# Performance work log

Hardware: AMD Instinct MI355X
Metric: run time of the kernel (lower is better)

## Reference

```python
import jax, jax.numpy as jnp
import numpy as np

TAU = 0.2        # temperature
LAM = 0.5        # lambda_weight
P = 128          # proj_dim


def l2n(x):
    # tf.math.l2_normalize semantics: x / sqrt(max(sum(x^2), eps))
    return x / jnp.sqrt(jnp.maximum(jnp.sum(x * x, axis=-1, keepdims=True), 1e-12))


def global_head(feat, W1, b1, W2, b2):
    # GlobalAveragePooling2D -> Dense(2048, relu) -> Dense(128); dropout is identity in eval
    g = jnp.mean(feat, axis=(1, 2))                       # [B, C]
    return jax.nn.relu(g @ W1 + b1) @ W2 + b2             # [B, 128]


def dense_head(feat, W1, b1, W2, b2):
    # 1x1 Conv2D(2048, relu) -> 1x1 Conv2D(128) == per-pixel matmuls
    h = jax.nn.relu(jnp.einsum('bhwc,cd->bhwd', feat, W1) + b1)
    return jnp.einsum('bhwd,de->bhwe', h, W2) + b2        # [B, H, W, 128]


def dense_correspondence(q, k):
    b, h, w, c = q.shape
    f1 = q.reshape(b, h * w, c)
    f2 = k.reshape(b, h * w, c)
    sim = jnp.einsum('bnc,bmc->bnm', f1, f2)              # [B, hw, hw]
    idx = jnp.argmax(sim, axis=-1)                        # [B, hw]
    return jnp.take_along_axis(f2, idx[:, :, None], axis=1)  # batched gather


def info_nce(q, k):
    logits = (q @ k.T) / TAU                              # [N, N]
    lse = jax.nn.logsumexp(logits, axis=-1)
    pos = jnp.diagonal(logits)                            # labels = arange(N)
    return jnp.mean(lse - pos)


def queue_info_nce(q, k, queue):
    l_pos = jnp.sum(q * k, axis=-1, keepdims=True)        # [B, 1]
    l_neg = q @ queue.T                                   # [B, Q]
    logits = jnp.concatenate([l_pos, l_neg], axis=1) / TAU
    # labels are all zero -> positive logit is column 0
    return jnp.mean(jax.nn.logsumexp(logits, axis=-1) - logits[:, 0])


def setup_inputs() -> dict:
    key = jax.random.key(0)
    ks = jax.random.split(key, 16)
    B, H, W, C, D = 8, 28, 28, 1024, 2048
    Q = 65536
    s1 = 0.02
    inp = {
        'feat_q': jax.random.normal(ks[0], (B, H, W, C), jnp.float32),
        'feat_k': jax.random.normal(ks[1], (B, H, W, C), jnp.float32),
        'Wg1': jax.random.normal(ks[2], (C, D), jnp.float32) * s1,
        'bg1': jnp.zeros((D,), jnp.float32),
        'Wg2': jax.random.normal(ks[3], (D, P), jnp.float32) * s1,
        'bg2': jnp.zeros((P,), jnp.float32),
        'Wd1': jax.random.normal(ks[4], (C, D), jnp.float32) * s1,
        'bd1': jnp.zeros((D,), jnp.float32),
        'Wd2': jax.random.normal(ks[5], (D, P), jnp.float32) * s1,
        'bd2': jnp.zeros((P,), jnp.float32),
        'mWg1': jax.random.normal(ks[6], (C, D), jnp.float32) * s1,
        'mbg1': jnp.zeros((D,), jnp.float32),
        'mWg2': jax.random.normal(ks[7], (D, P), jnp.float32) * s1,
        'mbg2': jnp.zeros((P,), jnp.float32),
        'mWd1': jax.random.normal(ks[8], (C, D), jnp.float32) * s1,
        'mbd1': jnp.zeros((D,), jnp.float32),
        'mWd2': jax.random.normal(ks[9], (D, P), jnp.float32) * s1,
        'mbd2': jnp.zeros((P,), jnp.float32),
        'queue': l2n(jax.random.normal(ks[10], (Q, P), jnp.float32)),
    }
    return inp


def reference(feat_q, feat_k, Wg1, bg1, Wg2, bg2, Wd1, bd1, Wd2, bd2,
              mWg1, mbg1, mWg2, mbg2, mWd1, mbd1, mWd2, mbd2, queue):
    # student branch
    q_g = l2n(global_head(feat_q, Wg1, bg1, Wg2, bg2))
    q_d = l2n(dense_head(feat_q, Wd1, bd1, Wd2, bd2))
    # momentum (teacher) branch, stop-gradient as in train_step
    k_g = jax.lax.stop_gradient(l2n(global_head(feat_k, mWg1, mbg1, mWg2, mbg2)))
    k_d = jax.lax.stop_gradient(l2n(dense_head(feat_k, mWd1, mbd1, mWd2, mbd2)))
    # post-warmup path (warmup_epochs=0)
    l_g = queue_info_nce(q_g, k_g, queue)
    matched_k = dense_correspondence(q_d, k_d)
    l_d = info_nce(q_d.reshape(-1, P), matched_k.reshape(-1, P))
    total = (1.0 - LAM) * l_g + LAM * l_d
    return total
```

## Files before the change

### kernel.cpp

```cpp
#include <hip/hip_runtime.h>
#include <cstdint>

#define TAU_INV 5.0f
#define L2E 1.4426950408889634f

using ushort = unsigned short;
typedef __attribute__((ext_vector_type(8))) short s16x8;
typedef __attribute__((ext_vector_type(4))) float f32x4;

static __device__ __forceinline__ ushort f2bf(float x) {
  unsigned u = __float_as_uint(x);
  return (ushort)((u + 0x7fffu + ((u >> 16) & 1u)) >> 16);
}

static __device__ __forceinline__ float fexp2(float x) {
#if __has_builtin(__builtin_amdgcn_exp2f)
  return __builtin_amdgcn_exp2f(x);
#else
  return exp2f(x);
#endif
}

static __device__ __forceinline__ void gload_lds16(const void* g, void* l) {
  __builtin_amdgcn_global_load_lds(
      reinterpret_cast<const __attribute__((address_space(1))) void*>(
          reinterpret_cast<uintptr_t>(g)),
      reinterpret_cast<__attribute__((address_space(3))) void*>(
          (unsigned)reinterpret_cast<uintptr_t>(l)),
      16, 0, 0);
}

static __device__ __forceinline__ void xcd_swizzle(int gx, int gy, int& bx, int& by) {
  int nwg = gx * gy;
  int flat = by * gx + bx;
  int q = nwg >> 3, r = nwg & 7;
  int xcd = flat & 7, sl = flat >> 3;
  int tile = (xcd < r ? xcd * (q + 1) : r * (q + 1) + (xcd - r) * q) + sl;
  by = tile / gx;
  bx = tile - by * gx;
}

__global__ void k_cvt_pool(const float* __restrict__ feat, ushort* __restrict__ obf,
                           float* __restrict__ gpart) {
  int b = blockIdx.y, pc = blockIdx.x, t = threadIdx.x;
  const float* fp = feat + ((size_t)b * 784 + (size_t)pc * 7) * 1024;
  ushort* op = obf + ((size_t)b * 784 + (size_t)pc * 7) * 1024;
  float4 acc = {0.f, 0.f, 0.f, 0.f};
#pragma unroll
  for (int p = 0; p < 7; ++p) {
    float4 v = ((const float4*)(fp + (size_t)p * 1024))[t];
    acc.x += v.x; acc.y += v.y; acc.z += v.z; acc.w += v.w;
    ushort4 r;
    r.x = f2bf(v.x); r.y = f2bf(v.y); r.z = f2bf(v.z); r.w = f2bf(v.w);
    ((ushort4*)(op + (size_t)p * 1024))[t] = r;
  }
  ((float4*)(gpart + ((size_t)b * 112 + pc) * 1024))[t] = acc;
}

__global__ void k_gpool_fin(const float* __restrict__ gpart, float* __restrict__ g) {
  int idx = blockIdx.x * 256 + threadIdx.x;
  int b = idx >> 10, c = idx & 1023;
  float s = 0.f;
#pragma unroll 4
  for (int pc = 0; pc < 112; ++pc) s += gpart[((size_t)b * 112 + pc) * 1024 + c];
  g[idx] = s * (1.0f / 784.0f);
}

__global__ void k_dense1_part(const float* __restrict__ g, const float* __restrict__ W,
                              float* __restrict__ part1) {
  int d = blockIdx.x * 256 + threadIdx.x;
  int k0 = blockIdx.y * 64;
  __shared__ float gs[512];
  for (int i = threadIdx.x; i < 512; i += 256) gs[i] = g[(i >> 6) * 1024 + k0 + (i & 63)];
  __syncthreads();
  float acc[8] = {};
  for (int kk = 0; kk < 64; ++kk) {
    float w = W[(size_t)(k0 + kk) * 2048 + d];
#pragma unroll
    for (int b = 0; b < 8; ++b) acc[b] += gs[b * 64 + kk] * w;
  }
#pragma unroll
  for (int b = 0; b < 8; ++b) part1[((size_t)blockIdx.y * 8 + b) * 2048 + d] = acc[b];
}

__global__ void k_dense1_fin(const float* __restrict__ part1, const float* __restrict__ bias,
                             float* __restrict__ h) {
  int idx = blockIdx.x * 256 + threadIdx.x;
  int b = idx >> 11, d = idx & 2047;
  float s = bias[d];
#pragma unroll
  for (int ks = 0; ks < 16; ++ks) s += part1[((size_t)ks * 8 + b) * 2048 + d];
  h[idx] = fmaxf(s, 0.f);
}

__global__ void k_dense2_part(const float* __restrict__ h, const float* __restrict__ W2,
                              float* __restrict__ part2) {
  int d = threadIdx.x;
  int k0 = blockIdx.x * 64;
  __shared__ float hs[512];
  for (int i = threadIdx.x; i < 512; i += 128) hs[i] = h[(i >> 6) * 2048 + k0 + (i & 63)];
  __syncthreads();
  float acc[8] = {};
  for (int kk = 0; kk < 64; ++kk) {
    float w = W2[(size_t)(k0 + kk) * 128 + d];
#pragma unroll
    for (int b = 0; b < 8; ++b) acc[b] += hs[b * 64 + kk] * w;
  }
#pragma unroll
  for (int b = 0; b < 8; ++b) part2[((size_t)blockIdx.x * 8 + b) * 128 + d] = acc[b];
}

__global__ void k_head_fin(const float* __restrict__ p2q, const float* __restrict__ p2k,
                           const float* __restrict__ bq, const float* __restrict__ bk,
                           float* __restrict__ qg, float* __restrict__ kg,
                           float* __restrict__ lpos) {
  int b = blockIdx.x, lane = threadIdx.x;
  float q0 = bq[lane], q1 = bq[lane + 64];
  float k0 = bk[lane], k1 = bk[lane + 64];
#pragma unroll
  for (int s = 0; s < 32; ++s) {
    size_t base = ((size_t)s * 8 + b) * 128;
    q0 += p2q[base + lane]; q1 += p2q[base + lane + 64];
    k0 += p2k[base + lane]; k1 += p2k[base + lane + 64];
  }
  float sq = q0 * q0 + q1 * q1, sk = k0 * k0 + k1 * k1;
#pragma unroll
  for (int d = 1; d < 64; d <<= 1) { sq += __shfl_xor(sq, d); sk += __shfl_xor(sk, d); }
  float rq = 1.0f / sqrtf(fmaxf(sq, 1e-12f));
  float rk = 1.0f / sqrtf(fmaxf(sk, 1e-12f));
  q0 *= rq; q1 *= rq; k0 *= rk; k1 *= rk;
  qg[b * 128 + lane] = q0; qg[b * 128 + 64 + lane] = q1;
  kg[b * 128 + lane] = k0; kg[b * 128 + 64 + lane] = k1;
  float lp = q0 * k0 + q1 * k1;
#pragma unroll
  for (int d = 1; d < 64; d <<= 1) lp += __shfl_xor(lp, d);
  if (lane == 0) lpos[b] = lp;
}

__global__ void k_transpose_cvt(const float* __restrict__ W, ushort* __restrict__ Wt, int K, int N) {
  __shared__ float tile[32][33];
  int n0 = blockIdx.x * 32, k0 = blockIdx.y * 32;
  int tx = threadIdx.x & 31, ty = threadIdx.x >> 5;
#pragma unroll
  for (int i = 0; i < 32; i += 8)
    tile[ty + i][tx] = W[(size_t)(k0 + ty + i) * N + n0 + tx];
  __syncthreads();
#pragma unroll
  for (int i = 0; i < 32; i += 8)
    Wt[(size_t)(n0 + ty + i) * K + k0 + tx] = f2bf(tile[tx][ty + i]);
}

template <int EPI>
__global__ __launch_bounds__(256) void k_gemm_abt(
    const ushort* __restrict__ A, const ushort* __restrict__ B,
    const float* __restrict__ bias, void* __restrict__ o0, void* __restrict__ o1,
    int Mvalid, int Nvalid, int Kloop, int lda, int ldb, int ldOut, int ntiles,
    float scale, long sA, long sB) {
  __shared__ unsigned char smem[65536];
  const int tid = threadIdx.x;
  int bx = blockIdx.x, by = blockIdx.y;
  const int bz = blockIdx.z;
  xcd_swizzle(gridDim.x, gridDim.y, bx, by);
  const ushort* Ab = A + (size_t)bz * sA;
  const ushort* Bb = B + (size_t)bz * sB;
  const int mBase = by * 128, nBase = bx * 128;
  const int lane = tid & 63;
  const int wid = tid >> 6;
  const int wid_u = __builtin_amdgcn_readfirstlane(wid);
  const int wm = wid >> 1, wn = wid & 1;
  const int lg = lane >> 4, li = lane & 15;
  const int lrow = lane >> 3, lchunk = lane & 7;

  const ushort* aSrc[4];
  const ushort* bSrc[4];
  int ldsOff[4];
#pragma unroll
  for (int j = 0; j < 4; ++j) {
    int r = wid_u * 32 + j * 8 + lrow;
    int gc = (lchunk ^ lrow) << 3;
    int ga = mBase + r; ga = ga < Mvalid ? ga : Mvalid - 1;
    int gb = nBase + r; gb = gb < Nvalid ? gb : Nvalid - 1;
    aSrc[j] = Ab + (size_t)ga * lda + gc;
    bSrc[j] = Bb + (size_t)gb * ldb + gc;
    ldsOff[j] = (wid_u * 32 + j * 8) * 128;
  }
  f32x4 acc[4][4] = {};

  auto STAGE = [&](int buf, int k0) {
    unsigned base = (unsigned)buf * 32768u;
#pragma unroll
    for (int j = 0; j < 4; ++j) {
      gload_lds16(aSrc[j] + k0, smem + base + ldsOff[j]);
      gload_lds16(bSrc[j] + k0, smem + base + 16384 + ldsOff[j]);
    }
  };

  const int nt = Kloop >> 6;
  STAGE(0, 0);
  __syncthreads();
  for (int t = 0; t < nt; ++t) {
    if (t + 1 < nt) STAGE((t + 1) & 1, (t + 1) << 6);
    const unsigned char* As = smem + (t & 1) * 32768;
    const unsigned char* Bs = As + 16384;
#pragma unroll
    for (int ks = 0; ks < 2; ++ks) {
      s16x8 af[4], bfr[4];
#pragma unroll
      for (int mi = 0; mi < 4; ++mi) {
        int r = wm * 64 + mi * 16 + li;
        af[mi] = *(const s16x8*)(const void*)(As + r * 128 + ((ks * 64 + lg * 16) ^ ((r & 7) << 4)));
      }
#pragma unroll
      for (int ni = 0; ni < 4; ++ni) {
        int c = wn * 64 + ni * 16 + li;
        bfr[ni] = *(const s16x8*)(const void*)(Bs + c * 128 + ((ks * 64 + lg * 16) ^ ((c & 7) << 4)));
      }
#pragma unroll
      for (int mi = 0; mi < 4; ++mi)
#pragma unroll
        for (int ni = 0; ni < 4; ++ni)
          acc[mi][ni] = __builtin_amdgcn_mfma_f32_16x16x32_bf16(af[mi], bfr[ni], acc[mi][ni], 0, 0, 0);
    }
    __syncthreads();
  }

  if constexpr (EPI == 0 || EPI == 4) {
    bool full = (mBase + 128 <= Mvalid) && (nBase + 128 <= Nvalid);
    if (full) {
#pragma unroll
      for (int ni = 0; ni < 4; ++ni) {
        int c = nBase + wn * 64 + ni * 16 + li;
        float bv = (EPI == 0) ? bias[c] : 0.f;
#pragma unroll
        for (int mi = 0; mi < 4; ++mi) {
#pragma unroll
          for (int rg = 0; rg < 4; ++rg) {
            int r = mBase + wm * 64 + mi * 16 + lg * 4 + rg;
            if constexpr (EPI == 0) {
              float v = fmaxf(acc[mi][ni][rg] + bv, 0.f);
              ((ushort*)o0)[(size_t)r * ldOut + c] = f2bf(v);
            } else {
              ((float*)o0)[(size_t)bz * ntiles + (size_t)r * ldOut + c] = acc[mi][ni][rg];
            }
          }
        }
      }
    } else {
#pragma unroll
      for (int mi = 0; mi < 4; ++mi)
#pragma unroll
        for (int ni = 0; ni < 4; ++ni) {
          int c = nBase + wn * 64 + ni * 16 + li;
#pragma unroll
          for (int rg = 0; rg < 4; ++rg) {
            int r = mBase + wm * 64 + mi * 16 + lg * 4 + rg;
            if (r < Mvalid && c < Nvalid) {
              if constexpr (EPI == 0) {
                float v = fmaxf(acc[mi][ni][rg] + bias[c], 0.f);
                ((ushort*)o0)[(size_t)r * ldOut + c] = f2bf(v);
              } else {
                ((float*)o0)[(size_t)bz * ntiles + (size_t)r * ldOut + c] = acc[mi][ni][rg];
              }
            }
          }
        }
    }
  } else if constexpr (EPI == 2) {
    __syncthreads();
    float* reds = (float*)(void*)smem;
#pragma unroll
    for (int mi = 0; mi < 4; ++mi)
#pragma unroll
      for (int rg = 0; rg < 4; ++rg) {
        float s = fexp2(acc[mi][0][rg] * scale) + fexp2(acc[mi][1][rg] * scale) +
                  fexp2(acc[mi][2][rg] * scale) + fexp2(acc[mi][3][rg] * scale);
#pragma unroll
        for (int d = 1; d < 16; d <<= 1) s += __shfl_xor(s, d);
        int rl = wm * 64 + mi * 16 + lg * 4 + rg;
        if (li == 0) reds[rl * 2 + wn] = s;
      }
    __syncthreads();
    if (tid < 128) {
      size_t idx = (size_t)(mBase + tid) * ntiles + bx;
      ((float*)o0)[idx] = reds[tid * 2] + reds[tid * 2 + 1];
    }
  } else if constexpr (EPI == 3) {
    __syncthreads();
    float* redv = (float*)(void*)smem;
    int* redi = (int*)(void*)(smem + 1024);
#pragma unroll
    for (int mi = 0; mi < 4; ++mi)
#pragma unroll
      for (int rg = 0; rg < 4; ++rg) {
        float bv = -3.4e38f;
        int bi = 0x7fffffff;
#pragma unroll
        for (int ni = 0; ni < 4; ++ni) {
          int c = nBase + wn * 64 + ni * 16 + li;
          float v = (c < Nvalid) ? acc[mi][ni][rg] : -3.4e38f;
          if (v > bv || (v == bv && c < bi)) { bv = v; bi = c; }
        }
#pragma unroll
        for (int d = 1; d < 16; d <<= 1) {
          float ov = __shfl_xor(bv, d);
          int oi = __shfl_xor(bi, d);
          if (ov > bv || (ov == bv && oi < bi)) { bv = ov; bi = oi; }
        }
        int rl = wm * 64 + mi * 16 + lg * 4 + rg;
        if (li == 0) { redv[rl * 2 + wn] = bv; redi[rl * 2 + wn] = bi; }
      }
    __syncthreads();
    if (tid < 128) {
      int r = mBase + tid;
      if (r < Mvalid) {
        float v0 = redv[tid * 2], v1 = redv[tid * 2 + 1];
        int i0 = redi[tid * 2], i1 = redi[tid * 2 + 1];
        float v = v0; int bi2 = i0;
        if (v1 > v || (v1 == v && i1 < bi2)) { v = v1; bi2 = i1; }
        size_t idx = (size_t)(bz * Mvalid + r) * ntiles + bx;
        ((float*)o0)[idx] = v;
        ((int*)o1)[idx] = bi2;
      }
    }
  }
}

__global__ void k_l2n_rows(const float* __restrict__ part, const float* __restrict__ bias,
                           float* __restrict__ of, ushort* __restrict__ ob, int rows) {
  int row = blockIdx.x * 4 + (threadIdx.x >> 6);
  int lane = threadIdx.x & 63;
  if (row >= rows) return;
  size_t i0 = (size_t)row * 128 + lane;
  const size_t SL = 802816;
  float v0 = bias[lane]      + part[i0]      + part[SL + i0]      + part[2 * SL + i0]      + part[3 * SL + i0];
  float v1 = bias[lane + 64] + part[i0 + 64] + part[SL + i0 + 64] + part[2 * SL + i0 + 64] + part[3 * SL + i0 + 64];
  float ss = v0 * v0 + v1 * v1;
#pragma unroll
  for (int d = 1; d < 64; d <<= 1) ss += __shfl_xor(ss, d);
  float r = 1.0f / sqrtf(fmaxf(ss, 1e-12f));
  of[i0] = v0 * r;
  of[i0 + 64] = v1 * r;
  ob[i0] = f2bf(v0 * r);
  ob[i0 + 64] = f2bf(v1 * r);
}

__global__ void k_argmax_gather(const float* __restrict__ pval, const int* __restrict__ pidx,
                                const ushort* __restrict__ kd_bf, ushort* __restrict__ matched_bf,
                                int* __restrict__ idxf) {
  int n = blockIdx.x;
  int b = n / 784;
  float bv = pval[(size_t)n * 7];
  int bi = pidx[(size_t)n * 7];
#pragma unroll
  for (int t = 1; t < 7; ++t) {
    float v = pval[(size_t)n * 7 + t];
    int i2 = pidx[(size_t)n * 7 + t];
    if (v > bv) { bv = v; bi = i2; }
  }
  int lane = threadIdx.x;
  if (lane == 0) idxf[n] = bi;
  const ushort* src = kd_bf + (size_t)(b * 784 + bi) * 128;
  ushort* dst = matched_bf + (size_t)n * 128;
  dst[lane] = src[lane];
  dst[lane + 64] = src[lane + 64];
}

__global__ __launch_bounds__(256) void k_queue_nce(const float* __restrict__ queue,
                                                   const float* __restrict__ qg,
                                                   float* __restrict__ ps) {
  __shared__ float qs[1024];
  int tid = threadIdx.x;
  for (int i = tid; i < 1024; i += 256) qs[i] = qg[i];
  __syncthreads();
  int r = blockIdx.x * 256 + tid;
  const float* qr = queue + (size_t)r * 128;
  float a[8] = {0, 0, 0, 0, 0, 0, 0, 0};
  for (int j = 0; j < 128; j += 4) {
    float4 v = *(const float4*)(const void*)(qr + j);
#pragma unroll
    for (int b = 0; b < 8; ++b)
      a[b] += v.x * qs[b * 128 + j] + v.y * qs[b * 128 + j + 1] +
              v.z * qs[b * 128 + j + 2] + v.w * qs[b * 128 + j + 3];
  }
  __shared__ float lssum[8][4];
  int lane = tid & 63, w = tid >> 6;
#pragma unroll
  for (int b = 0; b < 8; ++b) {
    float s = fexp2(a[b] * (TAU_INV * L2E));
#pragma unroll
    for (int d = 1; d < 64; d <<= 1) s += __shfl_xor(s, d);
    if (lane == 0) lssum[b][w] = s;
  }
  __syncthreads();
  if (tid < 8) {
    int b = tid;
    ps[blockIdx.x * 8 + b] = lssum[b][0] + lssum[b][1] + lssum[b][2] + lssum[b][3];
  }
}

__global__ void k_row_lse(const float* __restrict__ psum, const int* __restrict__ idxf,
                          const float* __restrict__ qd, const float* __restrict__ kd,
                          float* __restrict__ diff) {
  int n = blockIdx.x * 4 + (threadIdx.x >> 6);
  int lane = threadIdx.x & 63;
  float s = (lane < 49) ? psum[(size_t)n * 49 + lane] : 0.f;
#pragma unroll
  for (int d = 1; d < 64; d <<= 1) s += __shfl_xor(s, d);
  int b = n / 784;
  int mr = b * 784 + idxf[n];
  float pos = qd[(size_t)n * 128 + lane] * kd[(size_t)mr * 128 + lane] +
              qd[(size_t)n * 128 + 64 + lane] * kd[(size_t)mr * 128 + 64 + lane];
#pragma unroll
  for (int d = 1; d < 64; d <<= 1) pos += __shfl_xor(pos, d);
  if (lane == 0) diff[n] = logf(s) - pos * TAU_INV;
}

__global__ void k_final(const float* __restrict__ ps, const float* __restrict__ lpos,
                        const float* __restrict__ diff, float* __restrict__ out) {
  int tid = threadIdx.x;
  int lane = tid & 63, w = tid >> 6;
  __shared__ float sm[4];
  float lg = 0.f;
  for (int b = 0; b < 8; ++b) {
    float s = ps[tid * 8 + b];
#pragma unroll
    for (int d = 1; d < 64; d <<= 1) s += __shfl_xor(s, d);
    if (lane == 0) sm[w] = s;
    __syncthreads();
    if (tid == 0) {
      float S = sm[0] + sm[1] + sm[2] + sm[3];
      float lp = lpos[b] * TAU_INV;
      S += fexp2(lp * L2E);
      lg += logf(S) - lp;
    }
    __syncthreads();
  }
  float v = 0.f;
  for (int i = tid; i < 6272; i += 256) v += diff[i];
#pragma unroll
  for (int d = 1; d < 64; d <<= 1) v += __shfl_xor(v, d);
  if (lane == 0) sm[w] = v;
  __syncthreads();
  if (tid == 0) {
    float ld = sm[0] + sm[1] + sm[2] + sm[3];
    out[0] = 0.5f * (lg * 0.125f) + 0.5f * (ld * (1.0f / 6272.0f));
  }
}

extern "C" void kernel_launch(void* const* d_in, const int* in_sizes, int n_in,
                              void* d_out, int out_size, void* d_ws, size_t ws_size,
                              hipStream_t stream) {
  (void)in_sizes; (void)n_in; (void)out_size; (void)ws_size;
  const float* feat_q = (const float*)d_in[0];
  const float* feat_k = (const float*)d_in[1];
  const float* Wg1 = (const float*)d_in[2];
  const float* bg1 = (const float*)d_in[3];
  const float* Wg2 = (const float*)d_in[4];
  const float* bg2 = (const float*)d_in[5];
  const float* Wd1 = (const float*)d_in[6];
  const float* bd1 = (const float*)d_in[7];
  const float* Wd2 = (const float*)d_in[8];
  const float* bd2 = (const float*)d_in[9];
  const float* mWg1 = (const float*)d_in[10];
  const float* mbg1 = (const float*)d_in[11];
  const float* mWg2 = (const float*)d_in[12];
  const float* mbg2 = (const float*)d_in[13];
  const float* mWd1 = (const float*)d_in[14];
  const float* mbd1 = (const float*)d_in[15];
  const float* mWd2 = (const float*)d_in[16];
  const float* mbd2 = (const float*)d_in[17];
  const float* queue = (const float*)d_in[18];
  float* out = (float*)d_out;

  char* ws = (char*)d_ws;
  size_t off = 0;
  auto alloc = [&](size_t bytes) -> void* {
    void* p = (void*)(ws + off);
    off += (bytes + 255) & ~(size_t)255;
    return p;
  };

  ushort* featq_bf = (ushort*)alloc(6272ull * 1024 * 2);
  ushort* featk_bf = (ushort*)alloc(6272ull * 1024 * 2);
  ushort* Wd1t = (ushort*)alloc(2048ull * 1024 * 2);
  ushort* mWd1t = (ushort*)alloc(2048ull * 1024 * 2);
  ushort* Wd2t = (ushort*)alloc(128ull * 2048 * 2);
  ushort* mWd2t = (ushort*)alloc(128ull * 2048 * 2);
  ushort* h_bf = (ushort*)alloc(6272ull * 2048 * 2);
  float* e2part = (float*)alloc(4ull * 6272 * 128 * 4);
  float* qd = (float*)alloc(6272ull * 128 * 4);
  float* kd = (float*)alloc(6272ull * 128 * 4);
  ushort* qd_bf = (ushort*)alloc(6272ull * 128 * 2);
  ushort* kd_bf = (ushort*)alloc(6272ull * 128 * 2);
  ushort* matched_bf = (ushort*)alloc(6272ull * 128 * 2);
  float* psum = (float*)alloc(6272ull * 49 * 4);
  float* pval = (float*)alloc(6272ull * 7 * 4);
  int* pidx = (int*)alloc(6272ull * 7 * 4);
  int* idxf = (int*)alloc(6272ull * 4);
  float* gpart = (float*)alloc(8ull * 112 * 1024 * 4);
  float* gq = (float*)alloc(8ull * 1024 * 4);
  float* gk = (float*)alloc(8ull * 1024 * 4);
  float* part1 = (float*)alloc(16ull * 8 * 2048 * 4);
  float* hgq = (float*)alloc(8ull * 2048 * 4);
  float* hgk = (float*)alloc(8ull * 2048 * 4);
  float* part2q = (float*)alloc(32ull * 8 * 128 * 4);
  float* part2k = (float*)alloc(32ull * 8 * 128 * 4);
  float* qg = (float*)alloc(8ull * 128 * 4);
  float* kg = (float*)alloc(8ull * 128 * 4);
  float* l_pos = (float*)alloc(8ull * 4);
  float* qpart_s = (float*)alloc(256ull * 8 * 4);
  float* diff = (float*)alloc(6272ull * 4);

  k_cvt_pool<<<dim3(112, 8), 256, 0, stream>>>(feat_q, featq_bf, gpart);
  k_gpool_fin<<<32, 256, 0, stream>>>(gpart, gq);
  k_cvt_pool<<<dim3(112, 8), 256, 0, stream>>>(feat_k, featk_bf, gpart);
  k_gpool_fin<<<32, 256, 0, stream>>>(gpart, gk);

  k_transpose_cvt<<<dim3(64, 32), 256, 0, stream>>>(Wd1, Wd1t, 1024, 2048);
  k_transpose_cvt<<<dim3(64, 32), 256, 0, stream>>>(mWd1, mWd1t, 1024, 2048);
  k_transpose_cvt<<<dim3(4, 64), 256, 0, stream>>>(Wd2, Wd2t, 2048, 128);
  k_transpose_cvt<<<dim3(4, 64), 256, 0, stream>>>(mWd2, mWd2t, 2048, 128);

  k_dense1_part<<<dim3(8, 16), 256, 0, stream>>>(gq, Wg1, part1);
  k_dense1_fin<<<64, 256, 0, stream>>>(part1, bg1, hgq);
  k_dense2_part<<<32, 128, 0, stream>>>(hgq, Wg2, part2q);
  k_dense1_part<<<dim3(8, 16), 256, 0, stream>>>(gk, mWg1, part1);
  k_dense1_fin<<<64, 256, 0, stream>>>(part1, mbg1, hgk);
  k_dense2_part<<<32, 128, 0, stream>>>(hgk, mWg2, part2k);
  k_head_fin<<<8, 64, 0, stream>>>(part2q, part2k, bg2, mbg2, qg, kg, l_pos);

  k_gemm_abt<0><<<dim3(16, 49, 1), 256, 0, stream>>>(featq_bf, Wd1t, bd1, h_bf, nullptr,
                                                     6272, 2048, 1024, 1024, 1024, 2048, 0, 0.f, 0, 0);
  k_gemm_abt<4><<<dim3(1, 49, 4), 256, 0, stream>>>(h_bf, Wd2t, nullptr, e2part, nullptr,
                                                    6272, 128, 512, 2048, 2048, 128, 802816, 0.f, 512, 512);
  k_l2n_rows<<<1568, 256, 0, stream>>>(e2part, bd2, qd, qd_bf, 6272);

  k_gemm_abt<0><<<dim3(16, 49, 1), 256, 0, stream>>>(featk_bf, mWd1t, mbd1, h_bf, nullptr,
                                                     6272, 2048, 1024, 1024, 1024, 2048, 0, 0.f, 0, 0);
  k_gemm_abt<4><<<dim3(1, 49, 4), 256, 0, stream>>>(h_bf, mWd2t, nullptr, e2part, nullptr,
                                                    6272, 128, 512, 2048, 2048, 128, 802816, 0.f, 512, 512);
  k_l2n_rows<<<1568, 256, 0, stream>>>(e2part, mbd2, kd, kd_bf, 6272);

  k_gemm_abt<3><<<dim3(7, 7, 8), 256, 0, stream>>>(qd_bf, kd_bf, nullptr, pval, pidx,
                                                   784, 784, 128, 128, 128, 0, 7, 0.f,
                                                   784l * 128, 784l * 128);
  k_argmax_gather<<<6272, 64, 0, stream>>>(pval, pidx, kd_bf, matched_bf, idxf);

  k_gemm_abt<2><<<dim3(49, 49, 1), 256, 0, stream>>>(qd_bf, matched_bf, nullptr, psum, nullptr,
                                                     6272, 6272, 128, 128, 128, 0, 49,
                                                     TAU_INV * L2E, 0, 0);

  k_queue_nce<<<256, 256, 0, stream>>>(queue, qg, qpart_s);

  k_row_lse<<<1568, 256, 0, stream>>>(psum, idxf, qd, kd, diff);
  k_final<<<1, 256, 0, stream>>>(qpart_s, l_pos, diff, out);
}
```

Baseline: 270.4 us.

## Add 256x256-tile 8-wave GEMM for dense-head first layer

Replaces the 128x128 tiled GEMM for the two big dense-head first-layer matmuls (6272x2048x1024) with a new 256x256-tile kernel using 512 threads, 128KB dynamic LDS double buffering, and interleaved prefetch/MFMA phases with setprio. Larger tiles raise arithmetic intensity and reduce global/LDS traffic per FLOP, while staged A/B issue overlaps loads with compute. The grid drops to 200 blocks on a 256-CU part, so some CUs sit idle and the last M tile is partially wasted; heavy LDS use also limits occupancy.

Result: slower. 285.3 us (+5.5%).

```diff
diff --git a/kernel.cpp b/kernel.cpp
--- a/kernel.cpp
+++ b/kernel.cpp
@@ -148,6 +148,168 @@
 #pragma unroll
   for (int i = 0; i < 32; i += 8)
     Wt[(size_t)(n0 + ty + i) * K + k0 + tx] = f2bf(tile[tx][ty + i]);
+}
+
+__global__ __launch_bounds__(512, 2) void k_gemm256(
+    const ushort* __restrict__ A, const ushort* __restrict__ B,
+    const float* __restrict__ bias, ushort* __restrict__ O,
+    int Mvalid, int K, int ldOut) {
+  extern __shared__ unsigned char smem[];
+  const int tid = threadIdx.x;
+  int bx = blockIdx.x, by = blockIdx.y;
+  xcd_swizzle(gridDim.x, gridDim.y, bx, by);
+  const int mBase = by * 256, nBase = bx * 256;
+  const int lane = tid & 63;
+  const int wid_u = __builtin_amdgcn_readfirstlane(tid >> 6);
+  const int wm = wid_u >> 2, wn = wid_u & 3;
+  const int lg = lane >> 4, li = lane & 15;
+  const int lrow = lane >> 3, lchunk = lane & 7;
+  const int gc = (lchunk ^ lrow) << 3;
+  const int qb = wm * 2 + (wn & 1);
+  const int hB = wn >> 1;
+
+  const ushort* aSrc[4]; const ushort* bSrc[4];
+  unsigned aDst[4], bDst[4];
+#pragma unroll
+  for (int j = 0; j < 4; ++j) {
+    int r2a = wn * 32 + j * 8 + lrow;
+    int ga = mBase + wm * 128 + r2a; ga = ga < Mvalid ? ga : Mvalid - 1;
+    aSrc[j] = A + (size_t)ga * K + gc;
+    aDst[j] = (unsigned)(wm * 16384 + (wn * 32 + j * 8) * 128);
+    int r2b = qb * 32 + j * 8 + lrow;
+    int gb = nBase + hB * 128 + r2b;
+    bSrc[j] = B + (size_t)gb * K + gc;
+    bDst[j] = (unsigned)(32768 + hB * 16384 + (qb * 32 + j * 8) * 128);
+  }
+
+  f32x4 acc[8][4] = {};
+  const int nt = K >> 6;
+
+  auto ISSUE_A = [&](unsigned nb, int ko) {
+#pragma unroll
+    for (int j = 0; j < 4; ++j) gload_lds16(aSrc[j] + ko, smem + nb + aDst[j]);
+  };
+  auto ISSUE_B = [&](unsigned nb, int ko) {
+#pragma unroll
+    for (int j = 0; j < 4; ++j) gload_lds16(bSrc[j] + ko, smem + nb + bDst[j]);
+  };
+
+  ISSUE_A(0, 0); ISSUE_B(0, 0);
+  __syncthreads();
+
+  for (int t = 0; t < nt; ++t) {
+    const unsigned bb = (unsigned)(t & 1) * 65536u;
+    const unsigned nb = bb ^ 65536u;
+    const bool pf = (t + 1 < nt);
+    const int ko = (t + 1) << 6;
+    const unsigned char* Ah = smem + bb + wm * 16384;
+    const unsigned char* Bh = smem + bb + 32768 + hB * 16384;
+
+    s16x8 bf[4][2];
+    s16x8 af0[2][2], af1[2][2];
+
+    if (pf) ISSUE_A(nb, ko);
+#pragma unroll
+    for (int ni = 0; ni < 4; ++ni) {
+      int r2 = (wn & 1) * 64 + ni * 16 + li;
+#pragma unroll
+      for (int ks = 0; ks < 2; ++ks)
+        bf[ni][ks] = *(const s16x8*)(const void*)(Bh + r2 * 128 + (((ks * 4 + lg) ^ (r2 & 7)) << 4));
+    }
+#pragma unroll
+    for (int e = 0; e < 2; ++e) {
+      int r2 = e * 16 + li;
+#pragma unroll
+      for (int ks = 0; ks < 2; ++ks)
+        af0[e][ks] = *(const s16x8*)(const void*)(Ah + r2 * 128 + (((ks * 4 + lg) ^ (r2 & 7)) << 4));
+    }
+    __builtin_amdgcn_s_barrier();
+    __builtin_amdgcn_s_setprio(1);
+#pragma unroll
+    for (int e = 0; e < 2; ++e)
+#pragma unroll
+      for (int ni = 0; ni < 4; ++ni)
+#pragma unroll
+        for (int ks = 0; ks < 2; ++ks)
+          acc[e][ni] = __builtin_amdgcn_mfma_f32_16x16x32_bf16(af0[e][ks], bf[ni][ks], acc[e][ni], 0, 0, 0);
+    __builtin_amdgcn_s_setprio(0);
+    __builtin_amdgcn_s_barrier();
+
+    if (pf) ISSUE_B(nb, ko);
+#pragma unroll
+    for (int e = 0; e < 2; ++e) {
+      int r2 = (2 + e) * 16 + li;
+#pragma unroll
+      for (int ks = 0; ks < 2; ++ks)
+        af1[e][ks] = *(const s16x8*)(const void*)(Ah + r2 * 128 + (((ks * 4 + lg) ^ (r2 & 7)) << 4));
+    }
+    __builtin_amdgcn_s_barrier();
+    __builtin_amdgcn_s_setprio(1);
+#pragma unroll
+    for (int e = 0; e < 2; ++e)
+#pragma unroll
+      for (int ni = 0; ni < 4; ++ni)
+#pragma unroll
+        for (int ks = 0; ks < 2; ++ks)
+          acc[2 + e][ni] = __builtin_amdgcn_mfma_f32_16x16x32_bf16(af1[e][ks], bf[ni][ks], acc[2 + e][ni], 0, 0, 0);
+    __builtin_amdgcn_s_setprio(0);
+    __builtin_amdgcn_s_barrier();
+
+#pragma unroll
+    for (int e = 0; e < 2; ++e) {
+      int r2 = (4 + e) * 16 + li;
+#pragma unroll
+      for (int ks = 0; ks < 2; ++ks)
+        af0[e][ks] = *(const s16x8*)(const void*)(Ah + r2 * 128 + (((ks * 4 + lg) ^ (r2 & 7)) << 4));
+    }
+    __builtin_amdgcn_s_barrier();
+    __builtin_amdgcn_s_setprio(1);
+#pragma unroll
+    for (int e = 0; e < 2; ++e)
+#pragma unroll
+      for (int ni = 0; ni < 4; ++ni)
+#pragma unroll
+        for (int ks = 0; ks < 2; ++ks)
+          acc[4 + e][ni] = __builtin_amdgcn_mfma_f32_16x16x32_bf16(af0[e][ks], bf[ni][ks], acc[4 + e][ni], 0, 0, 0);
+    __builtin_amdgcn_s_setprio(0);
+    __builtin_amdgcn_s_barrier();
+
+#pragma unroll
+    for (int e = 0; e < 2; ++e) {
+      int r2 = (6 + e) * 16 + li;
+#pragma unroll
+      for (int ks = 0; ks < 2; ++ks)
+        af1[e][ks] = *(const s16x8*)(const void*)(Ah + r2 * 128 + (((ks * 4 + lg) ^ (r2 & 7)) << 4));
+    }
+    __builtin_amdgcn_s_barrier();
+    __builtin_amdgcn_s_setprio(1);
+#pragma unroll
+    for (int e = 0; e < 2; ++e)
+#pragma unroll
+      for (int ni = 0; ni < 4; ++ni)
+#pragma unroll
+        for (int ks = 0; ks < 2; ++ks)
+          acc[6 + e][ni] = __builtin_amdgcn_mfma_f32_16x16x32_bf16(af1[e][ks], bf[ni][ks], acc[6 + e][ni], 0, 0, 0);
+    __builtin_amdgcn_s_setprio(0);
+    __syncthreads();
+  }
+
+#pragma unroll
+  for (int ni = 0; ni < 4; ++ni) {
+    int c = nBase + wn * 64 + ni * 16 + li;
+    float bv = bias[c];
+#pragma unroll
+    for (int mi = 0; mi < 8; ++mi) {
+#pragma unroll
+      for (int rg = 0; rg < 4; ++rg) {
+        int r = mBase + wm * 128 + mi * 16 + lg * 4 + rg;
+        if (r < Mvalid) {
+          float v = fmaxf(acc[mi][ni][rg] + bv, 0.f);
+          O[(size_t)r * ldOut + c] = f2bf(v);
+        }
+      }
+    }
+  }
 }
 
 template <int EPI>
@@ -471,6 +633,9 @@
   const float* mbd2 = (const float*)d_in[17];
   const float* queue = (const float*)d_in[18];
   float* out = (float*)d_out;
+
+  (void)hipFuncSetAttribute(reinterpret_cast<const void*>(&k_gemm256),
+                            hipFuncAttributeMaxDynamicSharedMemorySize, 131072);
 
   char* ws = (char*)d_ws;
   size_t off = 0;
@@ -529,14 +694,12 @@
   k_dense2_part<<<32, 128, 0, stream>>>(hgk, mWg2, part2k);
   k_head_fin<<<8, 64, 0, stream>>>(part2q, part2k, bg2, mbg2, qg, kg, l_pos);
 
-  k_gemm_abt<0><<<dim3(16, 49, 1), 256, 0, stream>>>(featq_bf, Wd1t, bd1, h_bf, nullptr,
-                                                     6272, 2048, 1024, 1024, 1024, 2048, 0, 0.f, 0, 0);
+  k_gemm256<<<dim3(8, 25), 512, 131072, stream>>>(featq_bf, Wd1t, bd1, h_bf, 6272, 1024, 2048);
   k_gemm_abt<4><<<dim3(1, 49, 4), 256, 0, stream>>>(h_bf, Wd2t, nullptr, e2part, nullptr,
                                                     6272, 128, 512, 2048, 2048, 128, 802816, 0.f, 512, 512);
   k_l2n_rows<<<1568, 256, 0, stream>>>(e2part, bd2, qd, qd_bf, 6272);
 
-  k_gemm_abt<0><<<dim3(16, 49, 1), 256, 0, stream>>>(featk_bf, mWd1t, mbd1, h_bf, nullptr,
-                                                     6272, 2048, 1024, 1024, 1024, 2048, 0, 0.f, 0, 0);
+  k_gemm256<<<dim3(8, 25), 512, 131072, stream>>>(featk_bf, mWd1t, mbd1, h_bf, 6272, 1024, 2048);
   k_gemm_abt<4><<<dim3(1, 49, 4), 256, 0, stream>>>(h_bf, mWd2t, nullptr, e2part, nullptr,
                                                     6272, 128, 512, 2048, 2048, 128, 802816, 0.f, 512, 512);
   k_l2n_rows<<<1568, 256, 0, stream>>>(e2part, mbd2, kd, kd_bf, 6272);
```

## Batch student and teacher branches into shared launches and fuse head kernels

Applied to the files above, without the earlier changes.

Merges the query and key branches so each stage (convert/pool, weight transpose, global head, dense GEMMs, L2 normalisation) runs as a single launch over both branches via a grid z/y dimension. It also fuses the dense1 reduction with the dense2 partial products, and adds a specialised first-layer GEMM with no bounds checks. The aim is fewer launches and bigger grids that fill the GPU better, at the cost of twice the intermediate buffer memory, since h is no longer reused between branches.

Result: faster. 230.8 us (-14.7%).

```diff
diff --git a/kernel.cpp b/kernel.cpp
--- a/kernel.cpp
+++ b/kernel.cpp
@@ -40,11 +40,12 @@
   bx = tile - by * gx;
 }
 
-__global__ void k_cvt_pool(const float* __restrict__ feat, ushort* __restrict__ obf,
-                           float* __restrict__ gpart) {
-  int b = blockIdx.y, pc = blockIdx.x, t = threadIdx.x;
+__global__ void k_cvt_pool(const float* __restrict__ fq, const float* __restrict__ fk,
+                           ushort* __restrict__ obf, float* __restrict__ gpart) {
+  int br = blockIdx.y >> 3, b = blockIdx.y & 7, pc = blockIdx.x, t = threadIdx.x;
+  const float* feat = br ? fk : fq;
   const float* fp = feat + ((size_t)b * 784 + (size_t)pc * 7) * 1024;
-  ushort* op = obf + ((size_t)b * 784 + (size_t)pc * 7) * 1024;
+  ushort* op = obf + (size_t)br * 6422528 + ((size_t)b * 784 + (size_t)pc * 7) * 1024;
   float4 acc = {0.f, 0.f, 0.f, 0.f};
 #pragma unroll
   for (int p = 0; p < 7; ++p) {
@@ -54,24 +55,28 @@
     r.x = f2bf(v.x); r.y = f2bf(v.y); r.z = f2bf(v.z); r.w = f2bf(v.w);
     ((ushort4*)(op + (size_t)p * 1024))[t] = r;
   }
-  ((float4*)(gpart + ((size_t)b * 112 + pc) * 1024))[t] = acc;
+  ((float4*)(gpart + ((size_t)blockIdx.y * 112 + pc) * 1024))[t] = acc;
 }
 
 __global__ void k_gpool_fin(const float* __restrict__ gpart, float* __restrict__ g) {
   int idx = blockIdx.x * 256 + threadIdx.x;
-  int b = idx >> 10, c = idx & 1023;
+  int bb = idx >> 10, c = idx & 1023;
   float s = 0.f;
 #pragma unroll 4
-  for (int pc = 0; pc < 112; ++pc) s += gpart[((size_t)b * 112 + pc) * 1024 + c];
+  for (int pc = 0; pc < 112; ++pc) s += gpart[((size_t)bb * 112 + pc) * 1024 + c];
   g[idx] = s * (1.0f / 784.0f);
 }
 
-__global__ void k_dense1_part(const float* __restrict__ g, const float* __restrict__ W,
-                              float* __restrict__ part1) {
+__global__ void k_dense1_part(const float* __restrict__ g, const float* __restrict__ W0,
+                              const float* __restrict__ W1, float* __restrict__ part1) {
+  int br = blockIdx.z;
+  const float* gb = g + (size_t)br * 8192;
+  const float* W = br ? W1 : W0;
+  float* p1 = part1 + (size_t)br * 262144;
   int d = blockIdx.x * 256 + threadIdx.x;
   int k0 = blockIdx.y * 64;
   __shared__ float gs[512];
-  for (int i = threadIdx.x; i < 512; i += 256) gs[i] = g[(i >> 6) * 1024 + k0 + (i & 63)];
+  for (int i = threadIdx.x; i < 512; i += 256) gs[i] = gb[(i >> 6) * 1024 + k0 + (i & 63)];
   __syncthreads();
   float acc[8] = {};
   for (int kk = 0; kk < 64; ++kk) {
@@ -80,26 +85,27 @@
     for (int b = 0; b < 8; ++b) acc[b] += gs[b * 64 + kk] * w;
   }
 #pragma unroll
-  for (int b = 0; b < 8; ++b) part1[((size_t)blockIdx.y * 8 + b) * 2048 + d] = acc[b];
-}
-
-__global__ void k_dense1_fin(const float* __restrict__ part1, const float* __restrict__ bias,
-                             float* __restrict__ h) {
-  int idx = blockIdx.x * 256 + threadIdx.x;
-  int b = idx >> 11, d = idx & 2047;
-  float s = bias[d];
-#pragma unroll
-  for (int ks = 0; ks < 16; ++ks) s += part1[((size_t)ks * 8 + b) * 2048 + d];
-  h[idx] = fmaxf(s, 0.f);
-}
-
-__global__ void k_dense2_part(const float* __restrict__ h, const float* __restrict__ W2,
-                              float* __restrict__ part2) {
+  for (int b = 0; b < 8; ++b) p1[((size_t)blockIdx.y * 8 + b) * 2048 + d] = acc[b];
+}
+
+__global__ void k_d12(const float* __restrict__ part1, const float* __restrict__ b10,
+                      const float* __restrict__ b11, const float* __restrict__ W20,
+                      const float* __restrict__ W21, float* __restrict__ part2) {
+  int br = blockIdx.y, k0 = blockIdx.x * 64;
+  const float* p1 = part1 + (size_t)br * 262144;
+  const float* b1 = br ? b11 : b10;
+  const float* W2 = br ? W21 : W20;
+  float* p2 = part2 + (size_t)br * 32768;
+  __shared__ float hs[512];
+  for (int i = threadIdx.x; i < 512; i += 128) {
+    int b = i >> 6, kk = i & 63;
+    float s = b1[k0 + kk];
+#pragma unroll
+    for (int ks = 0; ks < 16; ++ks) s += p1[((size_t)ks * 8 + b) * 2048 + k0 + kk];
+    hs[i] = fmaxf(s, 0.f);
+  }
+  __syncthreads();
   int d = threadIdx.x;
-  int k0 = blockIdx.x * 64;
-  __shared__ float hs[512];
-  for (int i = threadIdx.x; i < 512; i += 128) hs[i] = h[(i >> 6) * 2048 + k0 + (i & 63)];
-  __syncthreads();
   float acc[8] = {};
   for (int kk = 0; kk < 64; ++kk) {
     float w = W2[(size_t)(k0 + kk) * 128 + d];
@@ -107,7 +113,7 @@
     for (int b = 0; b < 8; ++b) acc[b] += hs[b * 64 + kk] * w;
   }
 #pragma unroll
-  for (int b = 0; b < 8; ++b) part2[((size_t)blockIdx.x * 8 + b) * 128 + d] = acc[b];
+  for (int b = 0; b < 8; ++b) p2[((size_t)blockIdx.x * 8 + b) * 128 + d] = acc[b];
 }
 
 __global__ void k_head_fin(const float* __restrict__ p2q, const float* __restrict__ p2k,
@@ -137,7 +143,10 @@
   if (lane == 0) lpos[b] = lp;
 }
 
-__global__ void k_transpose_cvt(const float* __restrict__ W, ushort* __restrict__ Wt, int K, int N) {
+__global__ void k_transpose_cvt(const float* __restrict__ W0, const float* __restrict__ W1,
+                                ushort* __restrict__ Wt, int K, int N, size_t strideOut) {
+  const float* W = blockIdx.z ? W1 : W0;
+  ushort* o = Wt + (size_t)blockIdx.z * strideOut;
   __shared__ float tile[32][33];
   int n0 = blockIdx.x * 32, k0 = blockIdx.y * 32;
   int tx = threadIdx.x & 31, ty = threadIdx.x >> 5;
@@ -147,7 +156,95 @@
   __syncthreads();
 #pragma unroll
   for (int i = 0; i < 32; i += 8)
-    Wt[(size_t)(n0 + ty + i) * K + k0 + tx] = f2bf(tile[tx][ty + i]);
+    o[(size_t)(n0 + ty + i) * K + k0 + tx] = f2bf(tile[tx][ty + i]);
+}
+
+__global__ __launch_bounds__(256) void k_gemm_e1(
+    const ushort* __restrict__ A, long sA, const ushort* __restrict__ B, long sB,
+    const float* __restrict__ bias0, const float* __restrict__ bias1,
+    ushort* __restrict__ O, long sO, int K, int ldOut) {
+  __shared__ unsigned char smem[65536];
+  const int tid = threadIdx.x;
+  int bx = blockIdx.x, by = blockIdx.y;
+  const int bz = blockIdx.z;
+  xcd_swizzle(gridDim.x, gridDim.y, bx, by);
+  const ushort* Ab = A + (size_t)bz * sA;
+  const ushort* Bb = B + (size_t)bz * sB;
+  const float* bias = bz ? bias1 : bias0;
+  ushort* Ob = O + (size_t)bz * sO;
+  const int mBase = by * 128, nBase = bx * 128;
+  const int lane = tid & 63;
+  const int wid = tid >> 6;
+  const int wid_u = __builtin_amdgcn_readfirstlane(wid);
+  const int wm = wid >> 1, wn = wid & 1;
+  const int lg = lane >> 4, li = lane & 15;
+  const int lrow = lane >> 3, lchunk = lane & 7;
+
+  const ushort* aSrc[4];
+  const ushort* bSrc[4];
+  int ldsOff[4];
+#pragma unroll
+  for (int j = 0; j < 4; ++j) {
+    int r = wid_u * 32 + j * 8 + lrow;
+    int gc = (lchunk ^ lrow) << 3;
+    aSrc[j] = Ab + (size_t)(mBase + r) * K + gc;
+    bSrc[j] = Bb + (size_t)(nBase + r) * K + gc;
+    ldsOff[j] = (wid_u * 32 + j * 8) * 128;
+  }
+  f32x4 acc[4][4] = {};
+
+  auto STAGE = [&](int buf, int k0) {
+    unsigned base = (unsigned)buf * 32768u;
+#pragma unroll
+    for (int j = 0; j < 4; ++j) {
+      gload_lds16(aSrc[j] + k0, smem + base + ldsOff[j]);
+      gload_lds16(bSrc[j] + k0, smem + base + 16384 + ldsOff[j]);
+    }
+  };
+
+  const int nt = K >> 6;
+  STAGE(0, 0);
+  __syncthreads();
+  for (int t = 0; t < nt; ++t) {
+    if (t + 1 < nt) STAGE((t + 1) & 1, (t + 1) << 6);
+    const unsigned char* As = smem + (t & 1) * 32768;
+    const unsigned char* Bs = As + 16384;
+#pragma unroll
+    for (int ks = 0; ks < 2; ++ks) {
+      s16x8 af[4], bfr[4];
+#pragma unroll
+      for (int mi = 0; mi < 4; ++mi) {
+        int r = wm * 64 + mi * 16 + li;
+        af[mi] = *(const s16x8*)(const void*)(As + r * 128 + ((ks * 64 + lg * 16) ^ ((r & 7) << 4)));
+      }
+#pragma unroll
+      for (int ni = 0; ni < 4; ++ni) {
+        int c = wn * 64 + ni * 16 + li;
+        bfr[ni] = *(const s16x8*)(const void*)(Bs + c * 128 + ((ks * 64 + lg * 16) ^ ((c & 7) << 4)));
+      }
+#pragma unroll
+      for (int mi = 0; mi < 4; ++mi)
+#pragma unroll
+        for (int ni = 0; ni < 4; ++ni)
+          acc[mi][ni] = __builtin_amdgcn_mfma_f32_16x16x32_bf16(af[mi], bfr[ni], acc[mi][ni], 0, 0, 0);
+    }
+    __syncthreads();
+  }
+
+#pragma unroll
+  for (int ni = 0; ni < 4; ++ni) {
+    int c = nBase + wn * 64 + ni * 16 + li;
+    float bv = bias[c];
+#pragma unroll
+    for (int mi = 0; mi < 4; ++mi) {
+#pragma unroll
+      for (int rg = 0; rg < 4; ++rg) {
+        int r = mBase + wm * 64 + mi * 16 + lg * 4 + rg;
+        float v = fmaxf(acc[mi][ni][rg] + bv, 0.f);
+        Ob[(size_t)r * ldOut + c] = f2bf(v);
+      }
+    }
+  }
 }
 
 template <int EPI>
@@ -161,8 +258,15 @@
   int bx = blockIdx.x, by = blockIdx.y;
   const int bz = blockIdx.z;
   xcd_swizzle(gridDim.x, gridDim.y, bx, by);
-  const ushort* Ab = A + (size_t)bz * sA;
-  const ushort* Bb = B + (size_t)bz * sB;
+  const ushort* Ab;
+  const ushort* Bb;
+  if constexpr (EPI == 4) {
+    Ab = A + (size_t)(bz >> 2) * sA + (size_t)(bz & 3) * Kloop;
+    Bb = B + (size_t)(bz >> 2) * sB + (size_t)(bz & 3) * Kloop;
+  } else {
+    Ab = A + (size_t)bz * sA;
+    Bb = B + (size_t)bz * sB;
+  }
   const int mBase = by * 128, nBase = bx * 128;
   const int lane = tid & 63;
   const int wid = tid >> 6;
@@ -224,45 +328,17 @@
     __syncthreads();
   }
 
-  if constexpr (EPI == 0 || EPI == 4) {
-    bool full = (mBase + 128 <= Mvalid) && (nBase + 128 <= Nvalid);
-    if (full) {
-#pragma unroll
-      for (int ni = 0; ni < 4; ++ni) {
-        int c = nBase + wn * 64 + ni * 16 + li;
-        float bv = (EPI == 0) ? bias[c] : 0.f;
-#pragma unroll
-        for (int mi = 0; mi < 4; ++mi) {
-#pragma unroll
-          for (int rg = 0; rg < 4; ++rg) {
-            int r = mBase + wm * 64 + mi * 16 + lg * 4 + rg;
-            if constexpr (EPI == 0) {
-              float v = fmaxf(acc[mi][ni][rg] + bv, 0.f);
-              ((ushort*)o0)[(size_t)r * ldOut + c] = f2bf(v);
-            } else {
-              ((float*)o0)[(size_t)bz * ntiles + (size_t)r * ldOut + c] = acc[mi][ni][rg];
-            }
-          }
-        }
-      }
-    } else {
+  if constexpr (EPI == 4) {
+#pragma unroll
+    for (int ni = 0; ni < 4; ++ni) {
+      int c = nBase + wn * 64 + ni * 16 + li;
 #pragma unroll
       for (int mi = 0; mi < 4; ++mi)
 #pragma unroll
-        for (int ni = 0; ni < 4; ++ni) {
-          int c = nBase + wn * 64 + ni * 16 + li;
-#pragma unroll
-          for (int rg = 0; rg < 4; ++rg) {
-            int r = mBase + wm * 64 + mi * 16 + lg * 4 + rg;
-            if (r < Mvalid && c < Nvalid) {
-              if constexpr (EPI == 0) {
-                float v = fmaxf(acc[mi][ni][rg] + bias[c], 0.f);
-                ((ushort*)o0)[(size_t)r * ldOut + c] = f2bf(v);
-              } else {
-                ((float*)o0)[(size_t)bz * ntiles + (size_t)r * ldOut + c] = acc[mi][ni][rg];
-              }
-            }
-          }
+        for (int rg = 0; rg < 4; ++rg) {
+          int r = mBase + wm * 64 + mi * 16 + lg * 4 + rg;
+          if (r < Mvalid && c < Nvalid)
+            ((float*)o0)[(size_t)bz * ntiles + (size_t)r * ldOut + c] = acc[mi][ni][rg];
         }
     }
   } else if constexpr (EPI == 2) {
@@ -325,23 +401,28 @@
   }
 }
 
-__global__ void k_l2n_rows(const float* __restrict__ part, const float* __restrict__ bias,
-                           float* __restrict__ of, ushort* __restrict__ ob, int rows) {
+__global__ void k_l2n_rows(const float* __restrict__ part, const float* __restrict__ bias0,
+                           const float* __restrict__ bias1, float* __restrict__ of,
+                           ushort* __restrict__ ob) {
+  int br = blockIdx.y;
+  const float* p = part + (size_t)br * 3211264;
+  const float* bias = br ? bias1 : bias0;
+  float* o = of + (size_t)br * 802816;
+  ushort* o2 = ob + (size_t)br * 802816;
   int row = blockIdx.x * 4 + (threadIdx.x >> 6);
   int lane = threadIdx.x & 63;
-  if (row >= rows) return;
   size_t i0 = (size_t)row * 128 + lane;
   const size_t SL = 802816;
-  float v0 = bias[lane]      + part[i0]      + part[SL + i0]      + part[2 * SL + i0]      + part[3 * SL + i0];
-  float v1 = bias[lane + 64] + part[i0 + 64] + part[SL + i0 + 64] + part[2 * SL + i0 + 64] + part[3 * SL + i0 + 64];
+  float v0 = bias[lane]      + p[i0]      + p[SL + i0]      + p[2 * SL + i0]      + p[3 * SL + i0];
+  float v1 = bias[lane + 64] + p[i0 + 64] + p[SL + i0 + 64] + p[2 * SL + i0 + 64] + p[3 * SL + i0 + 64];
   float ss = v0 * v0 + v1 * v1;
 #pragma unroll
   for (int d = 1; d < 64; d <<= 1) ss += __shfl_xor(ss, d);
   float r = 1.0f / sqrtf(fmaxf(ss, 1e-12f));
-  of[i0] = v0 * r;
-  of[i0 + 64] = v1 * r;
-  ob[i0] = f2bf(v0 * r);
-  ob[i0 + 64] = f2bf(v1 * r);
+  o[i0] = v0 * r;
+  o[i0 + 64] = v1 * r;
+  o2[i0] = f2bf(v0 * r);
+  o2[i0 + 64] = f2bf(v1 * r);
 }
 
 __global__ void k_argmax_gather(const float* __restrict__ pval, const int* __restrict__ pidx,
@@ -480,78 +561,56 @@
     return p;
   };
 
-  ushort* featq_bf = (ushort*)alloc(6272ull * 1024 * 2);
-  ushort* featk_bf = (ushort*)alloc(6272ull * 1024 * 2);
-  ushort* Wd1t = (ushort*)alloc(2048ull * 1024 * 2);
-  ushort* mWd1t = (ushort*)alloc(2048ull * 1024 * 2);
-  ushort* Wd2t = (ushort*)alloc(128ull * 2048 * 2);
-  ushort* mWd2t = (ushort*)alloc(128ull * 2048 * 2);
-  ushort* h_bf = (ushort*)alloc(6272ull * 2048 * 2);
-  float* e2part = (float*)alloc(4ull * 6272 * 128 * 4);
-  float* qd = (float*)alloc(6272ull * 128 * 4);
-  float* kd = (float*)alloc(6272ull * 128 * 4);
-  ushort* qd_bf = (ushort*)alloc(6272ull * 128 * 2);
-  ushort* kd_bf = (ushort*)alloc(6272ull * 128 * 2);
+  ushort* feat_bf = (ushort*)alloc(2ull * 6272 * 1024 * 2);
+  ushort* Wd1t2 = (ushort*)alloc(2ull * 2048 * 1024 * 2);
+  ushort* Wd2t2 = (ushort*)alloc(2ull * 128 * 2048 * 2);
+  ushort* h_bf2 = (ushort*)alloc(2ull * 6272 * 2048 * 2);
+  float* e2part2 = (float*)alloc(2ull * 4 * 6272 * 128 * 4);
+  float* qdkd = (float*)alloc(2ull * 6272 * 128 * 4);
+  ushort* qdkd_bf = (ushort*)alloc(2ull * 6272 * 128 * 2);
   ushort* matched_bf = (ushort*)alloc(6272ull * 128 * 2);
   float* psum = (float*)alloc(6272ull * 49 * 4);
   float* pval = (float*)alloc(6272ull * 7 * 4);
   int* pidx = (int*)alloc(6272ull * 7 * 4);
   int* idxf = (int*)alloc(6272ull * 4);
-  float* gpart = (float*)alloc(8ull * 112 * 1024 * 4);
-  float* gq = (float*)alloc(8ull * 1024 * 4);
-  float* gk = (float*)alloc(8ull * 1024 * 4);
-  float* part1 = (float*)alloc(16ull * 8 * 2048 * 4);
-  float* hgq = (float*)alloc(8ull * 2048 * 4);
-  float* hgk = (float*)alloc(8ull * 2048 * 4);
-  float* part2q = (float*)alloc(32ull * 8 * 128 * 4);
-  float* part2k = (float*)alloc(32ull * 8 * 128 * 4);
+  float* gpart = (float*)alloc(16ull * 112 * 1024 * 4);
+  float* g2 = (float*)alloc(2ull * 8 * 1024 * 4);
+  float* part1 = (float*)alloc(2ull * 16 * 8 * 2048 * 4);
+  float* part2 = (float*)alloc(2ull * 32 * 8 * 128 * 4);
   float* qg = (float*)alloc(8ull * 128 * 4);
   float* kg = (float*)alloc(8ull * 128 * 4);
   float* l_pos = (float*)alloc(8ull * 4);
   float* qpart_s = (float*)alloc(256ull * 8 * 4);
   float* diff = (float*)alloc(6272ull * 4);
 
-  k_cvt_pool<<<dim3(112, 8), 256, 0, stream>>>(feat_q, featq_bf, gpart);
-  k_gpool_fin<<<32, 256, 0, stream>>>(gpart, gq);
-  k_cvt_pool<<<dim3(112, 8), 256, 0, stream>>>(feat_k, featk_bf, gpart);
-  k_gpool_fin<<<32, 256, 0, stream>>>(gpart, gk);
-
-  k_transpose_cvt<<<dim3(64, 32), 256, 0, stream>>>(Wd1, Wd1t, 1024, 2048);
-  k_transpose_cvt<<<dim3(64, 32), 256, 0, stream>>>(mWd1, mWd1t, 1024, 2048);
-  k_transpose_cvt<<<dim3(4, 64), 256, 0, stream>>>(Wd2, Wd2t, 2048, 128);
-  k_transpose_cvt<<<dim3(4, 64), 256, 0, stream>>>(mWd2, mWd2t, 2048, 128);
-
-  k_dense1_part<<<dim3(8, 16), 256, 0, stream>>>(gq, Wg1, part1);
-  k_dense1_fin<<<64, 256, 0, stream>>>(part1, bg1, hgq);
-  k_dense2_part<<<32, 128, 0, stream>>>(hgq, Wg2, part2q);
-  k_dense1_part<<<dim3(8, 16), 256, 0, stream>>>(gk, mWg1, part1);
-  k_dense1_fin<<<64, 256, 0, stream>>>(part1, mbg1, hgk);
-  k_dense2_part<<<32, 128, 0, stream>>>(hgk, mWg2, part2k);
-  k_head_fin<<<8, 64, 0, stream>>>(part2q, part2k, bg2, mbg2, qg, kg, l_pos);
-
-  k_gemm_abt<0><<<dim3(16, 49, 1), 256, 0, stream>>>(featq_bf, Wd1t, bd1, h_bf, nullptr,
-                                                     6272, 2048, 1024, 1024, 1024, 2048, 0, 0.f, 0, 0);
-  k_gemm_abt<4><<<dim3(1, 49, 4), 256, 0, stream>>>(h_bf, Wd2t, nullptr, e2part, nullptr,
-                                                    6272, 128, 512, 2048, 2048, 128, 802816, 0.f, 512, 512);
-  k_l2n_rows<<<1568, 256, 0, stream>>>(e2part, bd2, qd, qd_bf, 6272);
-
-  k_gemm_abt<0><<<dim3(16, 49, 1), 256, 0, stream>>>(featk_bf, mWd1t, mbd1, h_bf, nullptr,
-                                                     6272, 2048, 1024, 1024, 1024, 2048, 0, 0.f, 0, 0);
-  k_gemm_abt<4><<<dim3(1, 49, 4), 256, 0, stream>>>(h_bf, mWd2t, nullptr, e2part, nullptr,
-                                                    6272, 128, 512, 2048, 2048, 128, 802816, 0.f, 512, 512);
-  k_l2n_rows<<<1568, 256, 0, stream>>>(e2part, mbd2, kd, kd_bf, 6272);
-
-  k_gemm_abt<3><<<dim3(7, 7, 8), 256, 0, stream>>>(qd_bf, kd_bf, nullptr, pval, pidx,
+  k_cvt_pool<<<dim3(112, 16), 256, 0, stream>>>(feat_q, feat_k, feat_bf, gpart);
+  k_gpool_fin<<<64, 256, 0, stream>>>(gpart, g2);
+
+  k_transpose_cvt<<<dim3(64, 32, 2), 256, 0, stream>>>(Wd1, mWd1, Wd1t2, 1024, 2048, 2097152);
+  k_transpose_cvt<<<dim3(4, 64, 2), 256, 0, stream>>>(Wd2, mWd2, Wd2t2, 2048, 128, 262144);
+
+  k_dense1_part<<<dim3(8, 16, 2), 256, 0, stream>>>(g2, Wg1, mWg1, part1);
+  k_d12<<<dim3(32, 2), 128, 0, stream>>>(part1, bg1, mbg1, Wg2, mWg2, part2);
+  k_head_fin<<<8, 64, 0, stream>>>(part2, part2 + 32768, bg2, mbg2, qg, kg, l_pos);
+
+  k_gemm_e1<<<dim3(16, 49, 2), 256, 0, stream>>>(feat_bf, 6422528, Wd1t2, 2097152,
+                                                 bd1, mbd1, h_bf2, 12845056, 1024, 2048);
+  k_gemm_abt<4><<<dim3(1, 49, 8), 256, 0, stream>>>(h_bf2, Wd2t2, nullptr, e2part2, nullptr,
+                                                    6272, 128, 512, 2048, 2048, 128, 802816,
+                                                    0.f, 12845056, 262144);
+  k_l2n_rows<<<dim3(1568, 2), 256, 0, stream>>>(e2part2, bd2, mbd2, qdkd, qdkd_bf);
+
+  k_gemm_abt<3><<<dim3(7, 7, 8), 256, 0, stream>>>(qdkd_bf, qdkd_bf + 802816, nullptr, pval, pidx,
                                                    784, 784, 128, 128, 128, 0, 7, 0.f,
                                                    784l * 128, 784l * 128);
-  k_argmax_gather<<<6272, 64, 0, stream>>>(pval, pidx, kd_bf, matched_bf, idxf);
-
-  k_gemm_abt<2><<<dim3(49, 49, 1), 256, 0, stream>>>(qd_bf, matched_bf, nullptr, psum, nullptr,
+  k_argmax_gather<<<6272, 64, 0, stream>>>(pval, pidx, qdkd_bf + 802816, matched_bf, idxf);
+
+  k_gemm_abt<2><<<dim3(49, 49, 1), 256, 0, stream>>>(qdkd_bf, matched_bf, nullptr, psum, nullptr,
                                                      6272, 6272, 128, 128, 128, 0, 49,
                                                      TAU_INV * L2E, 0, 0);
 
   k_queue_nce<<<256, 256, 0, stream>>>(queue, qg, qpart_s);
 
-  k_row_lse<<<1568, 256, 0, stream>>>(psum, idxf, qd, kd, diff);
+  k_row_lse<<<1568, 256, 0, stream>>>(psum, idxf, qdkd, qdkd + 802816, diff);
   k_final<<<1, 256, 0, stream>>>(qpart_s, l_pos, diff, out);
 }
```
